# Optimization experiments

Measured on AMD Instinct MI355X. Metric: run time of the kernel, lower is better.

## Reference

```python
import jax, jax.numpy as jnp
import numpy as np

C_IN = 192
HEADS = 6
QKV_DIM = C_IN // HEADS  # 32
WH = WW = 4              # window_size
PAD_H = WH // 2          # 2
PAD_W = WW // 2          # 2


def setup_inputs() -> dict:
    key = jax.random.key(0)
    ks = jax.random.split(key, 6)
    s = 0.02
    return {
        "x": jax.random.normal(ks[0], (8, C_IN, 128, 128), jnp.float32),
        "w_qkv1": jax.random.normal(ks[1], (3 * C_IN, C_IN), jnp.float32) * s,
        "b_qkv1": jnp.zeros((3 * C_IN,), jnp.float32),
        "w_qkv2": jax.random.normal(ks[2], (3 * C_IN, C_IN), jnp.float32) * s,
        "b_qkv2": jnp.zeros((3 * C_IN,), jnp.float32),
        "w_head": jax.random.normal(ks[3], (C_IN, 2 * C_IN), jnp.float32) * s,  # 1x1 conv as matmul
        "b_head": jnp.zeros((C_IN,), jnp.float32),
    }


def _window_partition(x):
    # bchw_to_bnc: [B,C,H,W] -> [B*nh*nw, WH*WW, C]
    B, C, H, W = x.shape
    nh, nw = H // WH, W // WW
    x = x.reshape(B, C, nh, WH, nw, WW)
    x = x.transpose(0, 2, 4, 3, 5, 1)  # B,nh,nw,WH,WW,C
    return x.reshape(B * nh * nw, WH * WW, C)


def _window_merge(x, out_shape):
    # bnc_to_bchw: inverse of _window_partition
    B, C, H, W = out_shape
    nh, nw = H // WH, W // WW
    x = x.reshape(B, nh, nw, WH, WW, C)
    x = x.transpose(0, 5, 1, 3, 2, 4)  # B,C,nh,WH,nw,WW
    return x.reshape(B, C, H, W)


def _mha(xw, w, b):
    # xw: [Bn, N=16, C]; fused QKV projection then per-window SDPA
    Bn, N, C = xw.shape
    qkv = xw @ w.T + b
    q, k, v = jnp.split(qkv, 3, axis=-1)
    to_heads = lambda t: t.reshape(Bn, N, HEADS, QKV_DIM).transpose(0, 2, 1, 3)
    q, k, v = to_heads(q), to_heads(k), to_heads(v)
    scale = 1.0 / np.sqrt(QKV_DIM).astype(np.float32)
    attn = jax.nn.softmax(jnp.einsum('bhnd,bhmd->bhnm', q, k) * scale, axis=-1)
    o = jnp.einsum('bhnm,bhmd->bhnd', attn, v)
    return o.transpose(0, 2, 1, 3).reshape(Bn, N, C)


def reference(x, w_qkv1, b_qkv1, w_qkv2, b_qkv2, w_head, b_head):
    # branch 2: zero-pad by window//2 on each side (shifted windows)
    x2 = jnp.pad(x, ((0, 0), (0, 0), (PAD_H, PAD_H), (PAD_W, PAD_W)))
    s1, s2 = x.shape, x2.shape
    o1 = _window_merge(_mha(_window_partition(x), w_qkv1, b_qkv1), s1)
    o2 = _window_merge(_mha(_window_partition(x2), w_qkv2, b_qkv2), s2)
    o2 = o2[:, :, PAD_H:-PAD_H, PAD_W:-PAD_W]  # negative pad = crop
    o = jnp.concatenate([o1, o2], axis=1)      # [B, 2C, H, W]
    # 1x1 conv head projection
    return jnp.einsum('bchw,oc->bohw', o, w_head) + b_head[None, :, None, None]
```

## Files before the change

kernel.cpp:

```cpp
#include <hip/hip_runtime.h>


typedef unsigned short u16;
using bf16x8 = __attribute__((ext_vector_type(8))) short;
using f32x4  = __attribute__((ext_vector_type(4))) float;
using u16x8  = __attribute__((ext_vector_type(8))) unsigned short;
using u16x4  = __attribute__((ext_vector_type(4))) unsigned short;

#define CIN   192
#define CQKV  576
#define NW2   33

__device__ __forceinline__ float bf2f(u16 u) {
    unsigned int x = ((unsigned int)u) << 16;
    float f; __builtin_memcpy(&f, &x, 4); return f;
}
__device__ __forceinline__ u16 f2bf(float f) {
    unsigned int x; __builtin_memcpy(&x, &f, 4);
    return (u16)((x + 0x7FFFu + ((x >> 16) & 1u)) >> 16);
}
__device__ __forceinline__ int xcol(int c, int tok) {
    int blk = (c >> 3) ^ ((tok ^ (tok >> 4)) & 7);
    return blk * 8 + (c & 7);
}

__global__ void prep_conv(const float* __restrict__ w1, const float* __restrict__ w2,
                          const float* __restrict__ wh,
                          u16* __restrict__ w1b, u16* __restrict__ w2b, u16* __restrict__ whb) {
    int i = blockIdx.x * 256 + threadIdx.x;
    if (i < 110592)        w1b[i] = f2bf(w1[i]);
    else if (i < 221184)   w2b[i - 110592] = f2bf(w2[i - 110592]);
    else                   whb[i - 221184] = f2bf(wh[i - 221184]);
}

template<int BR>
__global__ __launch_bounds__(256, 2) void qkv_attn(const float* __restrict__ x,
                                                   const u16* __restrict__ wb,
                                                   const float* __restrict__ bias,
                                                   u16* __restrict__ ocat) {
    __shared__ __align__(16) char smem[77824];
    u16* xl = (u16*)smem;
    u16* wl = (u16*)(smem + 25600);
    u16* qk = (u16*)smem;
    u16* vt = (u16*)(smem + 50176);
    u16* pl = (u16*)(smem + 74752);

    const int tid  = threadIdx.x;
    const int wave = tid >> 6, lane = tid & 63;
    const int lo16 = lane & 15, quad = lane >> 4;

    int b, wy, g;
    if (BR == 0) {
        int bi = blockIdx.x;
        b = bi >> 8; int rem = bi & 255;
        wy = rem >> 3; g = rem & 7;
    } else {
        int bi = blockIdx.x;
        b = bi / 297; int rem = bi % 297;
        wy = rem / 9; g = rem % 9;
    }
    const int hbase = wy * 4, wbase = g * 16;

#pragma unroll
    for (int it = 0; it < 12; ++it) {
        int i = it * 256 + tid;
        int c = i >> 4, y = (i >> 2) & 3, xc = i & 3;
        float e0, e1, e2, e3;
        if (BR == 0) {
            const float4 v = *reinterpret_cast<const float4*>(
                &x[(((size_t)b * CIN + c) * 128 + hbase + y) * 128 + wbase + xc * 4]);
            e0 = v.x; e1 = v.y; e2 = v.z; e3 = v.w;
        } else {
            int h = hbase + y - 2;
            int w0 = wbase + xc * 4 - 2;
            bool hok = (unsigned)h < 128u;
            const float* row = &x[(((size_t)b * CIN + c) * 128 + h) * 128];
            if (hok && w0 >= 0 && w0 + 3 < 128) {
                float2 p0 = *reinterpret_cast<const float2*>(&row[w0]);
                float2 p1 = *reinterpret_cast<const float2*>(&row[w0 + 2]);
                e0 = p0.x; e1 = p0.y; e2 = p1.x; e3 = p1.y;
            } else {
                e0 = (hok && w0 >= 0 && w0 < 128)         ? row[w0]     : 0.f;
                e1 = (hok && w0+1 >= 0 && w0+1 < 128)     ? row[w0 + 1] : 0.f;
                e2 = (hok && w0+2 >= 0 && w0+2 < 128)     ? row[w0 + 2] : 0.f;
                e3 = (hok && w0+3 >= 0 && w0+3 < 128)     ? row[w0 + 3] : 0.f;
            }
        }
        int t0 = xc * 16 + y * 4;
        xl[(t0 + 0) * 200 + xcol(c, t0 + 0)] = f2bf(e0);
        xl[(t0 + 1) * 200 + xcol(c, t0 + 1)] = f2bf(e1);
        xl[(t0 + 2) * 200 + xcol(c, t0 + 2)] = f2bf(e2);
        xl[(t0 + 3) * 200 + xcol(c, t0 + 3)] = f2bf(e3);
    }
    __syncthreads();

    f32x4 acc[9][4];
#pragma unroll
    for (int mt = 0; mt < 9; ++mt)
#pragma unroll
        for (int nt = 0; nt < 4; ++nt) acc[mt][nt] = f32x4{0.f, 0.f, 0.f, 0.f};

    for (int s = 0; s < 6; ++s) {
#pragma unroll
        for (int it = 0; it < 9; ++it) {
            int i = it * 256 + tid;
            int co = i >> 2, kk = (i & 3) * 8;
            u16x8 v = *reinterpret_cast<const u16x8*>(&wb[co * 192 + s * 32 + kk]);
            *reinterpret_cast<u16x8*>(&wl[co * 40 + kk]) = v;
        }
        __syncthreads();
        bf16x8 bfr[4];
#pragma unroll
        for (int nt = 0; nt < 4; ++nt) {
            int tok = nt * 16 + lo16;
            int kb = s * 4 + quad;
            bfr[nt] = *reinterpret_cast<const bf16x8*>(
                &xl[tok * 200 + (((kb ^ ((tok ^ (tok >> 4)) & 7)) << 3))]);
        }
#pragma unroll
        for (int mt = 0; mt < 9; ++mt) {
            bf16x8 afr = *reinterpret_cast<const bf16x8*>(
                &wl[(wave * 144 + mt * 16 + lo16) * 40 + quad * 8]);
#pragma unroll
            for (int nt = 0; nt < 4; ++nt)
                acc[mt][nt] = __builtin_amdgcn_mfma_f32_16x16x32_bf16(afr, bfr[nt], acc[mt][nt], 0, 0, 0);
        }
        __syncthreads();
    }

    const float scale = 0.17677669529663687f;
#pragma unroll
    for (int mt = 0; mt < 9; ++mt) {
        int co0 = wave * 144 + mt * 16 + quad * 4;
        const float4 bv = *reinterpret_cast<const float4*>(&bias[co0]);
#pragma unroll
        for (int nt = 0; nt < 4; ++nt) {
            int tok = nt * 16 + lo16;
            float v0 = acc[mt][nt][0] + bv.x, v1 = acc[mt][nt][1] + bv.y;
            float v2 = acc[mt][nt][2] + bv.z, v3 = acc[mt][nt][3] + bv.w;
            if (co0 < 192) { v0 *= scale; v1 *= scale; v2 *= scale; v3 *= scale; }
            if (co0 < 384) {
                u16x4 pk = {f2bf(v0), f2bf(v1), f2bf(v2), f2bf(v3)};
                *reinterpret_cast<u16x4*>(&qk[tok * 392 + co0]) = pk;
            } else {
                int dh = co0 - 384;
                int head = dh >> 5, d0 = dh & 31;
                int win = tok >> 4, m = tok & 15;
                u16* vrow = &vt[((win * 6 + head) * 32 + d0) * 16 + m];
                vrow[0]  = f2bf(v0);
                vrow[16] = f2bf(v1);
                vrow[32] = f2bf(v2);
                vrow[48] = f2bf(v3);
            }
        }
    }
    __syncthreads();

    {
        const int win = wave;
        const u16* qbase = qk + (size_t)(win * 16) * 392;
        const bf16x8 z8 = {};
        const f32x4 zc = {0.f, 0.f, 0.f, 0.f};
        bool dov; size_t dst = 0;
        if (BR == 0) {
            int wg = wy * 32 + g * 4 + win;
            dst = (((size_t)(b * 1024 + wg)) * 16 + lo16) * 384;
            dov = true;
        } else {
            int wx = g * 4 + win;
            int h = wy * 4 + (lo16 >> 2) - 2;
            int w = wx * 4 + (lo16 & 3) - 2;
            dov = (wx < NW2) && (unsigned)h < 128u && (unsigned)w < 128u;
            if (dov) {
                int wg = (h >> 2) * 32 + (w >> 2);
                int nn = (h & 3) * 4 + (w & 3);
                dst = (((size_t)(b * 1024 + wg)) * 16 + nn) * 384 + 192;
            }
        }
#pragma unroll
        for (int head = 0; head < 6; ++head) {
            bf16x8 kfr = *reinterpret_cast<const bf16x8*>(
                &qbase[lo16 * 392 + 192 + head * 32 + quad * 8]);
            bf16x8 qfr = *reinterpret_cast<const bf16x8*>(
                &qbase[lo16 * 392 + head * 32 + quad * 8]);
            f32x4 st = __builtin_amdgcn_mfma_f32_16x16x32_bf16(kfr, qfr, zc, 0, 0, 0);
            float mx = fmaxf(fmaxf(st[0], st[1]), fmaxf(st[2], st[3]));
            mx = fmaxf(mx, __shfl_xor(mx, 16));
            mx = fmaxf(mx, __shfl_xor(mx, 32));
            float p0 = __expf(st[0] - mx), p1 = __expf(st[1] - mx);
            float p2 = __expf(st[2] - mx), p3 = __expf(st[3] - mx);
            float sum = p0 + p1 + p2 + p3;
            sum += __shfl_xor(sum, 16);
            sum += __shfl_xor(sum, 32);
            float inv = 1.0f / sum;
            u16x4 pk = {f2bf(p0), f2bf(p1), f2bf(p2), f2bf(p3)};
            *reinterpret_cast<u16x4*>(&pl[(wave * 16 + lo16) * 24 + quad * 4]) = pk;
            bf16x8 pf = (quad < 2)
                ? *reinterpret_cast<const bf16x8*>(&pl[(wave * 16 + lo16) * 24 + quad * 8]) : z8;
            const u16* vbase = &vt[(win * 6 + head) * 32 * 16];
#pragma unroll
            for (int half = 0; half < 2; ++half) {
                bf16x8 av = (quad < 2)
                    ? *reinterpret_cast<const bf16x8*>(&vbase[(half * 16 + lo16) * 16 + quad * 8]) : z8;
                f32x4 o = __builtin_amdgcn_mfma_f32_16x16x32_bf16(av, pf, zc, 0, 0, 0);
                if (dov) {
                    u16x4 ok = {f2bf(o[0] * inv), f2bf(o[1] * inv),
                                f2bf(o[2] * inv), f2bf(o[3] * inv)};
                    *reinterpret_cast<u16x4*>(&ocat[dst + head * 32 + half * 16 + quad * 4]) = ok;
                }
            }
        }
    }
}

__global__ __launch_bounds__(256, 3) void head_gemm(const u16* __restrict__ ocat,
                                                    const u16* __restrict__ whb,
                                                    const float* __restrict__ bh,
                                                    float* __restrict__ out) {
    __shared__ __align__(16) u16 bt[64 * 392];
    const int tid = threadIdx.x;
    const int wave = tid >> 6, lane = tid & 63;
    const int lo16 = lane & 15, quad = lane >> 4;

    int bi = blockIdx.x;
    int b = bi >> 8; int rem = bi & 255;
    int wy = rem >> 3, g = rem & 7;
    const int wg0 = wy * 32 + g * 4;
    const size_t gbase = ((size_t)(b * 1024 + wg0) * 16) * 384;

#pragma unroll
    for (int it = 0; it < 12; ++it) {
        int i = it * 256 + tid;
        u16x8 v = *reinterpret_cast<const u16x8*>(&ocat[gbase + (size_t)i * 8]);
        int row = i / 48, kc = i - row * 48;
        *reinterpret_cast<u16x8*>(&bt[row * 392 + kc * 8]) = v;
    }
    __syncthreads();

    const int co_base = wave * 48;
    f32x4 acc[3][4];
#pragma unroll
    for (int mt = 0; mt < 3; ++mt)
#pragma unroll
        for (int nt = 0; nt < 4; ++nt) acc[mt][nt] = f32x4{0.f, 0.f, 0.f, 0.f};

#pragma unroll
    for (int s = 0; s < 12; ++s) {
        int k0 = s * 32;
        bf16x8 a[3], bb[4];
#pragma unroll
        for (int nt = 0; nt < 4; ++nt)
            bb[nt] = *reinterpret_cast<const bf16x8*>(&bt[(nt * 16 + lo16) * 392 + k0 + quad * 8]);
#pragma unroll
        for (int mt = 0; mt < 3; ++mt)
            a[mt] = *reinterpret_cast<const bf16x8*>(
                &whb[(size_t)(co_base + mt * 16 + lo16) * 384 + k0 + quad * 8]);
#pragma unroll
        for (int mt = 0; mt < 3; ++mt)
#pragma unroll
            for (int nt = 0; nt < 4; ++nt)
                acc[mt][nt] = __builtin_amdgcn_mfma_f32_16x16x32_bf16(a[mt], bb[nt], acc[mt][nt], 0, 0, 0);
    }

    int h = wy * 4 + (lo16 >> 2);
#pragma unroll
    for (int mt = 0; mt < 3; ++mt) {
        int co0 = co_base + mt * 16 + quad * 4;
        const float4 bv = *reinterpret_cast<const float4*>(&bh[co0]);
#pragma unroll
        for (int r = 0; r < 4; ++r) {
            float bias = (r == 0) ? bv.x : (r == 1) ? bv.y : (r == 2) ? bv.z : bv.w;
#pragma unroll
            for (int nt = 0; nt < 4; ++nt) {
                int w = (g * 4 + nt) * 4 + (lo16 & 3);
                out[(((size_t)b * CIN + co0 + r) * 128 + h) * 128 + w] = acc[mt][nt][r] + bias;
            }
        }
    }
}

extern "C" void kernel_launch(void* const* d_in, const int* in_sizes, int n_in,
                              void* d_out, int out_size, void* d_ws, size_t ws_size,
                              hipStream_t stream) {
    const float* x  = (const float*)d_in[0];
    const float* w1 = (const float*)d_in[1];
    const float* b1 = (const float*)d_in[2];
    const float* w2 = (const float*)d_in[3];
    const float* b2 = (const float*)d_in[4];
    const float* wh = (const float*)d_in[5];
    const float* bh = (const float*)d_in[6];
    float* out = (float*)d_out;

    char* ws = (char*)d_ws;
    u16* ocat = (u16*)ws;
    u16* w1b  = (u16*)(ws + 100663296);
    u16* w2b  = (u16*)(ws + 100884480);
    u16* whb  = (u16*)(ws + 101105664);

    prep_conv<<<1152, 256, 0, stream>>>(w1, w2, wh, w1b, w2b, whb);
    qkv_attn<0><<<2048, 256, 0, stream>>>(x, w1b, b1, ocat);
    qkv_attn<1><<<2376, 256, 0, stream>>>(x, w2b, b2, ocat);
    head_gemm<<<2048, 256, 0, stream>>>(ocat, whb, bh, out);
}
```

Before: 454.7 us.

## Merge branch kernels, read QKV weights directly, shuffle softmax, vectorize head stores

The two templated attention launches become one 4424-block launch that picks the branch from the block index. QKV weight fragments are now read straight from global/L2 instead of being staged through shared memory, which removes six pairs of block barriers per tile. The P matrix is repacked with lane shuffles instead of an LDS round-trip. The head GEMM swaps its operand roles so each lane writes contiguous float4 outputs. The trade-offs are repeated global weight reads per wave, plus a fused kernel that has more branching and possibly higher register pressure.

```diff
diff --git a/kernel.cpp b/kernel.cpp
--- a/kernel.cpp
+++ b/kernel.cpp
@@ -7,14 +7,8 @@
 using u16x8  = __attribute__((ext_vector_type(8))) unsigned short;
 using u16x4  = __attribute__((ext_vector_type(4))) unsigned short;
 
-#define CIN   192
-#define CQKV  576
-#define NW2   33
-
-__device__ __forceinline__ float bf2f(u16 u) {
-    unsigned int x = ((unsigned int)u) << 16;
-    float f; __builtin_memcpy(&f, &x, 4); return f;
-}
+#define CIN 192
+
 __device__ __forceinline__ u16 f2bf(float f) {
     unsigned int x; __builtin_memcpy(&x, &f, 4);
     return (u16)((x + 0x7FFFu + ((x >> 16) & 1u)) >> 16);
@@ -33,32 +27,29 @@
     else                   whb[i - 221184] = f2bf(wh[i - 221184]);
 }
 
-template<int BR>
 __global__ __launch_bounds__(256, 2) void qkv_attn(const float* __restrict__ x,
-                                                   const u16* __restrict__ wb,
-                                                   const float* __restrict__ bias,
+                                                   const u16* __restrict__ w1b,
+                                                   const u16* __restrict__ w2b,
+                                                   const float* __restrict__ bias1,
+                                                   const float* __restrict__ bias2,
                                                    u16* __restrict__ ocat) {
-    __shared__ __align__(16) char smem[77824];
+    __shared__ __align__(16) char smem[74752];
     u16* xl = (u16*)smem;
-    u16* wl = (u16*)(smem + 25600);
     u16* qk = (u16*)smem;
     u16* vt = (u16*)(smem + 50176);
-    u16* pl = (u16*)(smem + 74752);
 
     const int tid  = threadIdx.x;
     const int wave = tid >> 6, lane = tid & 63;
     const int lo16 = lane & 15, quad = lane >> 4;
 
-    int b, wy, g;
-    if (BR == 0) {
-        int bi = blockIdx.x;
-        b = bi >> 8; int rem = bi & 255;
-        wy = rem >> 3; g = rem & 7;
+    int bi = blockIdx.x, BR, b, wy, g;
+    if (bi < 2048) {
+        BR = 0; b = bi >> 8; int rem = bi & 255; wy = rem >> 3; g = rem & 7;
     } else {
-        int bi = blockIdx.x;
-        b = bi / 297; int rem = bi % 297;
-        wy = rem / 9; g = rem % 9;
-    }
+        bi -= 2048; BR = 1; b = bi / 297; int rem = bi % 297; wy = rem / 9; g = rem % 9;
+    }
+    const u16*  wb   = BR ? w2b : w1b;
+    const float* bias = BR ? bias2 : bias1;
     const int hbase = wy * 4, wbase = g * 16;
 
 #pragma unroll
@@ -80,10 +71,10 @@
                 float2 p1 = *reinterpret_cast<const float2*>(&row[w0 + 2]);
                 e0 = p0.x; e1 = p0.y; e2 = p1.x; e3 = p1.y;
             } else {
-                e0 = (hok && w0 >= 0 && w0 < 128)         ? row[w0]     : 0.f;
-                e1 = (hok && w0+1 >= 0 && w0+1 < 128)     ? row[w0 + 1] : 0.f;
-                e2 = (hok && w0+2 >= 0 && w0+2 < 128)     ? row[w0 + 2] : 0.f;
-                e3 = (hok && w0+3 >= 0 && w0+3 < 128)     ? row[w0 + 3] : 0.f;
+                e0 = (hok && w0 >= 0 && w0 < 128)     ? row[w0]     : 0.f;
+                e1 = (hok && w0+1 >= 0 && w0+1 < 128) ? row[w0 + 1] : 0.f;
+                e2 = (hok && w0+2 >= 0 && w0+2 < 128) ? row[w0 + 2] : 0.f;
+                e3 = (hok && w0+3 >= 0 && w0+3 < 128) ? row[w0 + 3] : 0.f;
             }
         }
         int t0 = xc * 16 + y * 4;
@@ -100,33 +91,26 @@
 #pragma unroll
         for (int nt = 0; nt < 4; ++nt) acc[mt][nt] = f32x4{0.f, 0.f, 0.f, 0.f};
 
+#pragma unroll
     for (int s = 0; s < 6; ++s) {
-#pragma unroll
-        for (int it = 0; it < 9; ++it) {
-            int i = it * 256 + tid;
-            int co = i >> 2, kk = (i & 3) * 8;
-            u16x8 v = *reinterpret_cast<const u16x8*>(&wb[co * 192 + s * 32 + kk]);
-            *reinterpret_cast<u16x8*>(&wl[co * 40 + kk]) = v;
-        }
-        __syncthreads();
         bf16x8 bfr[4];
 #pragma unroll
         for (int nt = 0; nt < 4; ++nt) {
             int tok = nt * 16 + lo16;
             int kb = s * 4 + quad;
             bfr[nt] = *reinterpret_cast<const bf16x8*>(
-                &xl[tok * 200 + (((kb ^ ((tok ^ (tok >> 4)) & 7)) << 3))]);
+                &xl[tok * 200 + ((kb ^ ((tok ^ (tok >> 4)) & 7)) << 3)]);
         }
 #pragma unroll
         for (int mt = 0; mt < 9; ++mt) {
             bf16x8 afr = *reinterpret_cast<const bf16x8*>(
-                &wl[(wave * 144 + mt * 16 + lo16) * 40 + quad * 8]);
+                &wb[(size_t)(wave * 144 + mt * 16 + lo16) * 192 + s * 32 + quad * 8]);
 #pragma unroll
             for (int nt = 0; nt < 4; ++nt)
                 acc[mt][nt] = __builtin_amdgcn_mfma_f32_16x16x32_bf16(afr, bfr[nt], acc[mt][nt], 0, 0, 0);
         }
-        __syncthreads();
-    }
+    }
+    __syncthreads();
 
     const float scale = 0.17677669529663687f;
 #pragma unroll
@@ -161,6 +145,8 @@
         const u16* qbase = qk + (size_t)(win * 16) * 392;
         const bf16x8 z8 = {};
         const f32x4 zc = {0.f, 0.f, 0.f, 0.f};
+        const int sl0 = (quad & 1) * 32 + lo16;
+
         bool dov; size_t dst = 0;
         if (BR == 0) {
             int wg = wy * 32 + g * 4 + win;
@@ -170,7 +156,7 @@
             int wx = g * 4 + win;
             int h = wy * 4 + (lo16 >> 2) - 2;
             int w = wx * 4 + (lo16 & 3) - 2;
-            dov = (wx < NW2) && (unsigned)h < 128u && (unsigned)w < 128u;
+            dov = (wx < 33) && (unsigned)h < 128u && (unsigned)w < 128u;
             if (dov) {
                 int wg = (h >> 2) * 32 + (w >> 2);
                 int nn = (h & 3) * 4 + (w & 3);
@@ -193,11 +179,14 @@
             sum += __shfl_xor(sum, 16);
             sum += __shfl_xor(sum, 32);
             float inv = 1.0f / sum;
-            u16x4 pk = {f2bf(p0), f2bf(p1), f2bf(p2), f2bf(p3)};
-            *reinterpret_cast<u16x4*>(&pl[(wave * 16 + lo16) * 24 + quad * 4]) = pk;
-            bf16x8 pf = (quad < 2)
-                ? *reinterpret_cast<const bf16x8*>(&pl[(wave * 16 + lo16) * 24 + quad * 8]) : z8;
-            const u16* vbase = &vt[(win * 6 + head) * 32 * 16];
+            float f0 = __shfl(p0, sl0),      f1 = __shfl(p1, sl0);
+            float f2 = __shfl(p2, sl0),      f3 = __shfl(p3, sl0);
+            float f4 = __shfl(p0, sl0 + 16), f5 = __shfl(p1, sl0 + 16);
+            float f6 = __shfl(p2, sl0 + 16), f7 = __shfl(p3, sl0 + 16);
+            u16x8 pk = {f2bf(f0), f2bf(f1), f2bf(f2), f2bf(f3),
+                        f2bf(f4), f2bf(f5), f2bf(f6), f2bf(f7)};
+            bf16x8 pf = (quad < 2) ? *reinterpret_cast<bf16x8*>(&pk) : z8;
+            const u16* vbase = &vt[(win * 6 + head) * 512];
 #pragma unroll
             for (int half = 0; half < 2; ++half) {
                 bf16x8 av = (quad < 2)
@@ -225,8 +214,7 @@
     int bi = blockIdx.x;
     int b = bi >> 8; int rem = bi & 255;
     int wy = rem >> 3, g = rem & 7;
-    const int wg0 = wy * 32 + g * 4;
-    const size_t gbase = ((size_t)(b * 1024 + wg0) * 16) * 384;
+    const size_t gbase = ((size_t)(b * 1024 + wy * 32 + g * 4) * 16) * 384;
 
 #pragma unroll
     for (int it = 0; it < 12; ++it) {
@@ -237,44 +225,41 @@
     }
     __syncthreads();
 
-    const int co_base = wave * 48;
-    f32x4 acc[3][4];
-#pragma unroll
-    for (int mt = 0; mt < 3; ++mt)
-#pragma unroll
-        for (int nt = 0; nt < 4; ++nt) acc[mt][nt] = f32x4{0.f, 0.f, 0.f, 0.f};
+    f32x4 acc[4][3];
+#pragma unroll
+    for (int mt = 0; mt < 4; ++mt)
+#pragma unroll
+        for (int nt = 0; nt < 3; ++nt) acc[mt][nt] = f32x4{0.f, 0.f, 0.f, 0.f};
 
 #pragma unroll
     for (int s = 0; s < 12; ++s) {
         int k0 = s * 32;
-        bf16x8 a[3], bb[4];
-#pragma unroll
-        for (int nt = 0; nt < 4; ++nt)
-            bb[nt] = *reinterpret_cast<const bf16x8*>(&bt[(nt * 16 + lo16) * 392 + k0 + quad * 8]);
-#pragma unroll
-        for (int mt = 0; mt < 3; ++mt)
-            a[mt] = *reinterpret_cast<const bf16x8*>(
-                &whb[(size_t)(co_base + mt * 16 + lo16) * 384 + k0 + quad * 8]);
-#pragma unroll
-        for (int mt = 0; mt < 3; ++mt)
-#pragma unroll
-            for (int nt = 0; nt < 4; ++nt)
+        bf16x8 a[4], bb[3];
+#pragma unroll
+        for (int mt = 0; mt < 4; ++mt)
+            a[mt] = *reinterpret_cast<const bf16x8*>(&bt[(mt * 16 + lo16) * 392 + k0 + quad * 8]);
+#pragma unroll
+        for (int nt = 0; nt < 3; ++nt)
+            bb[nt] = *reinterpret_cast<const bf16x8*>(
+                &whb[(size_t)((wave * 3 + nt) * 16 + lo16) * 384 + k0 + quad * 8]);
+#pragma unroll
+        for (int mt = 0; mt < 4; ++mt)
+#pragma unroll
+            for (int nt = 0; nt < 3; ++nt)
                 acc[mt][nt] = __builtin_amdgcn_mfma_f32_16x16x32_bf16(a[mt], bb[nt], acc[mt][nt], 0, 0, 0);
     }
 
-    int h = wy * 4 + (lo16 >> 2);
-#pragma unroll
-    for (int mt = 0; mt < 3; ++mt) {
-        int co0 = co_base + mt * 16 + quad * 4;
-        const float4 bv = *reinterpret_cast<const float4*>(&bh[co0]);
-#pragma unroll
-        for (int r = 0; r < 4; ++r) {
-            float bias = (r == 0) ? bv.x : (r == 1) ? bv.y : (r == 2) ? bv.z : bv.w;
-#pragma unroll
-            for (int nt = 0; nt < 4; ++nt) {
-                int w = (g * 4 + nt) * 4 + (lo16 & 3);
-                out[(((size_t)b * CIN + co0 + r) * 128 + h) * 128 + w] = acc[mt][nt][r] + bias;
-            }
+    const int h = wy * 4 + quad;
+#pragma unroll
+    for (int nt = 0; nt < 3; ++nt) {
+        int co = (wave * 3 + nt) * 16 + lo16;
+        float bias = bh[co];
+#pragma unroll
+        for (int mt = 0; mt < 4; ++mt) {
+            float4 v = {acc[mt][nt][0] + bias, acc[mt][nt][1] + bias,
+                        acc[mt][nt][2] + bias, acc[mt][nt][3] + bias};
+            *reinterpret_cast<float4*>(
+                &out[(((size_t)b * CIN + co) * 128 + h) * 128 + (g * 4 + mt) * 4]) = v;
         }
     }
 }
@@ -298,7 +283,6 @@
     u16* whb  = (u16*)(ws + 101105664);
 
     prep_conv<<<1152, 256, 0, stream>>>(w1, w2, wh, w1b, w2b, whb);
-    qkv_attn<0><<<2048, 256, 0, stream>>>(x, w1b, b1, ocat);
-    qkv_attn<1><<<2376, 256, 0, stream>>>(x, w2b, b2, ocat);
+    qkv_attn<<<4424, 256, 0, stream>>>(x, w1b, w2b, b1, b2, ocat);
     head_gemm<<<2048, 256, 0, stream>>>(ocat, whb, bh, out);
 }
```

New measurement: 493.6 us. +8.6%, slower.
